# Kernel tuning notes

Measured on AMD Instinct MI355X. Metric: run time of the kernel, lower is better.

Reference implementation:

```python
import jax, jax.numpy as jnp
import numpy as np

N_NODES = 30000
N_EDGES = 480000
IN_CH, NF, OUT_CH = 64, 128, 3
N_HIDDEN = 6  # GCN(num_layers=7): conv0 (in->nf) + 6 convs (nf->nf)
SLOPE = 0.02


def setup_inputs() -> dict:
    key = jax.random.key(0)
    ks = jax.random.split(key, 8)
    x = jax.random.normal(ks[0], (N_NODES, IN_CH), dtype=jnp.float32)
    edge_index = jax.random.randint(ks[1], (2, N_EDGES), 0, N_NODES, dtype=jnp.int64)
    W0 = jax.random.normal(ks[2], (IN_CH, NF), dtype=jnp.float32) * (1.0 / np.sqrt(IN_CH))
    b0 = jnp.zeros((NF,), dtype=jnp.float32)
    Wh = jax.random.normal(ks[3], (N_HIDDEN, NF, NF), dtype=jnp.float32) * (1.0 / np.sqrt(NF))
    bh = jnp.zeros((N_HIDDEN, NF), dtype=jnp.float32)
    Wout = jax.random.normal(ks[4], (NF, OUT_CH), dtype=jnp.float32) * (1.0 / np.sqrt(NF))
    bout = jnp.zeros((OUT_CH,), dtype=jnp.float32)
    return {"x": x, "edge_index": edge_index, "W0": W0, "b0": b0,
            "Wh": Wh, "bh": bh, "Wout": Wout, "bout": bout}


def _gcn_norm(edge_index, n):
    # PyG GCNConv default: add self-loops, symmetric normalization D^-1/2 (A+I) D^-1/2
    loop = jnp.arange(n, dtype=edge_index.dtype)
    src = jnp.concatenate([edge_index[0], loop])
    dst = jnp.concatenate([edge_index[1], loop])
    deg = jax.ops.segment_sum(jnp.ones_like(dst, dtype=jnp.float32), dst, num_segments=n)
    dinv = jax.lax.rsqrt(deg)  # deg >= 1 due to self-loops
    norm = dinv[src] * dinv[dst]  # [E+N]
    return src, dst, norm


def _gcn_conv(h, W, b, src, dst, norm, n):
    h = h @ W                                   # [N, F_out]
    msg = h[src] * norm[:, None]                # gather + scale  [E+N, F_out]
    out = jax.ops.segment_sum(msg, dst, num_segments=n)  # scatter-add
    return out + b


def reference(x, edge_index, W0, b0, Wh, bh, Wout, bout):
    n = x.shape[0]
    src, dst, norm = _gcn_norm(edge_index, n)
    # 7-layer GCN stack with LeakyReLU(0.02) between layers; dropout is
    # identity in eval mode (training=False).
    h = _gcn_conv(x, W0, b0, src, dst, norm, n)
    for i in range(N_HIDDEN):
        h = jax.nn.leaky_relu(h, SLOPE)
        h = _gcn_conv(h, Wh[i], bh[i], src, dst, norm, n)
    # outer forward: leaky_relu -> dropout(eval=identity) -> out conv -> tanh*0.5
    h = jax.nn.leaky_relu(h, SLOPE)
    h = _gcn_conv(h, Wout, bout, src, dst, norm, n)
    return jnp.tanh(h) * 0.5
```

## Files before the change

kernel.cpp:

```cpp
#include <hip/hip_runtime.h>
#include <hip/hip_fp16.h>
#include <math.h>

#define NN 30000
#define NE 480000
#define NB 118
#define SCALE 512.0f
#define INVSCALE (1.0f / 512.0f)

typedef _Float16 half8 __attribute__((ext_vector_type(8)));
typedef float floatx4 __attribute__((ext_vector_type(4)));

__device__ __forceinline__ float lrelu(float v) { return v > 0.0f ? v : v * 0.02f; }

__device__ __forceinline__ float4 fma4(float4 v, float w, float4 a) {
    a.x = fmaf(v.x, w, a.x);
    a.y = fmaf(v.y, w, a.y);
    a.z = fmaf(v.z, w, a.z);
    a.w = fmaf(v.w, w, a.w);
    return a;
}

__device__ __forceinline__ float4 loadh4(const __half* p) {
    uint2 raw = *(const uint2*)p;
    __half2 h0 = *(__half2*)&raw.x;
    __half2 h1 = *(__half2*)&raw.y;
    float2 f0 = __half22float2(h0);
    float2 f1 = __half22float2(h1);
    return make_float4(f0.x, f0.y, f1.x, f1.y);
}


__global__ void k_count(const int* __restrict__ ei, int* __restrict__ cnt,
                        const float* __restrict__ W0, const float* __restrict__ Wh,
                        const float* __restrict__ b0, const float* __restrict__ bh,
                        __half* __restrict__ W0t, __half* __restrict__ Wht,
                        float* __restrict__ bs) {
    int g = blockIdx.x * 256 + threadIdx.x;
    if (g < NE) atomicAdd(&cnt[ei[NE + g]], 1);
    if (g < 8192) {
        int k = g >> 7, n = g & 127;
        W0t[n * 64 + k] = __float2half(W0[g] * SCALE);
    } else if (g < 8192 + 98304) {
        int j = g - 8192;
        int l = j >> 14;
        int r = j & 16383;
        int k = r >> 7, n = r & 127;
        Wht[l * 16384 + n * 128 + k] = __float2half(Wh[j]);
    } else if (g < 8192 + 98304 + 896) {
        int j = g - 8192 - 98304;
        bs[j] = (j < 128 ? b0[j] : bh[j - 128]) * SCALE;
    }
}

__global__ void k_scan1(const int* __restrict__ cnt, int* __restrict__ bsum,
                        float* __restrict__ dinv) {
    __shared__ int sd[256];
    int tid = threadIdx.x;
    int i = blockIdx.x * 256 + tid;
    int v = (i < NN) ? cnt[i] : 0;
    if (i < NN) dinv[i] = 1.0f / sqrtf((float)(v + 1));
    sd[tid] = v;
    __syncthreads();
    for (int off = 128; off > 0; off >>= 1) {
        if (tid < off) sd[tid] += sd[tid + off];
        __syncthreads();
    }
    if (tid == 0) bsum[blockIdx.x] = sd[0];
}

__global__ void k_scan3(const int* __restrict__ cnt, const int* __restrict__ bsum,
                        int* __restrict__ row_ptr, int* __restrict__ cursor) {
    __shared__ int sd[256];
    __shared__ int offs[128];
    int tid = threadIdx.x;
    if (tid < 128) offs[tid] = (tid < blockIdx.x) ? bsum[tid] : 0;
    __syncthreads();
    for (int o = 64; o > 0; o >>= 1) {
        if (tid < o) offs[tid] += offs[tid + o];
        __syncthreads();
    }
    int i = blockIdx.x * 256 + tid;
    int v = (i < NN) ? cnt[i] : 0;
    sd[tid] = v;
    __syncthreads();
    for (int off = 1; off < 256; off <<= 1) {
        int t = (tid >= off) ? sd[tid - off] : 0;
        __syncthreads();
        sd[tid] += t;
        __syncthreads();
    }
    if (i < NN) {
        int excl = offs[0] + sd[tid] - v;
        row_ptr[i] = excl;
        cursor[i] = excl;
        if (i == NN - 1) row_ptr[NN] = excl + v;
    }
}

__global__ void k_fill(const int* __restrict__ ei, const float* __restrict__ dinv,
                       int* __restrict__ cursor, int2* __restrict__ csr) {
    int e = blockIdx.x * 256 + threadIdx.x;
    if (e < NE) {
        int s = ei[e];
        int d = ei[NE + e];
        int pos = atomicAdd(&cursor[d], 1);
        float w = dinv[s] * dinv[d];
        csr[pos] = make_int2(s, __float_as_int(w));
    }
}


__launch_bounds__(512)
__global__ void k_layer0(const float* __restrict__ x, const int* __restrict__ row_ptr,
                         const int2* __restrict__ csr, const float* __restrict__ dinv,
                         const __half* __restrict__ Wt, const float* __restrict__ bias,
                         __half* __restrict__ out16) {
    __shared__ _Float16 hsF[2 * 4 * 16 * 8];
    int tid = threadIdx.x;
    int node0 = blockIdx.x * 16;
    {
        int nl = tid >> 5;
        int node = node0 + nl;
        int c = (tid & 31) * 2;
        float di = dinv[node];
        float w0 = di * di;
        float2 hv = *(const float2*)&x[(size_t)node * 64 + c];
        float2 acc[8];
        acc[0] = make_float2(hv.x * w0, hv.y * w0);
        #pragma unroll
        for (int j = 1; j < 8; j++) acc[j] = make_float2(0.f, 0.f);
        int e = row_ptr[node];
        int e1 = row_ptr[node + 1];
        for (; e + 8 <= e1; e += 8) {
            int2 sw[8];
            #pragma unroll
            for (int j = 0; j < 8; j++) sw[j] = csr[e + j];
            float2 v[8];
            #pragma unroll
            for (int j = 0; j < 8; j++) v[j] = *(const float2*)&x[(size_t)sw[j].x * 64 + c];
            #pragma unroll
            for (int j = 0; j < 8; j++) {
                float w = __int_as_float(sw[j].y);
                acc[j].x = fmaf(v[j].x, w, acc[j].x);
                acc[j].y = fmaf(v[j].y, w, acc[j].y);
            }
        }
        for (; e < e1; ++e) {
            int2 sw = csr[e];
            float2 v = *(const float2*)&x[(size_t)sw.x * 64 + c];
            float w = __int_as_float(sw.y);
            acc[0].x = fmaf(v.x, w, acc[0].x);
            acc[0].y = fmaf(v.y, w, acc[0].y);
        }
        #pragma unroll
        for (int j = 1; j < 8; j++) { acc[0].x += acc[j].x; acc[0].y += acc[j].y; }
        int ks = c >> 5, quad = (c >> 3) & 3, jj = c & 7;
        __half2 p = __floats2half2_rn(acc[0].x, acc[0].y);
        *(__half2*)&hsF[((ks * 4 + quad) * 16 + nl) * 8 + jj] = p;
    }
    __syncthreads();
    int wave = tid >> 6, lane = tid & 63, quad = lane >> 4, ln = lane & 15;
    half8 afrag[2];
    #pragma unroll
    for (int ks = 0; ks < 2; ks++)
        afrag[ks] = *(const half8*)&hsF[((ks * 4 + quad) * 16 + ln) * 8];
    floatx4 acc = (floatx4){0.f, 0.f, 0.f, 0.f};
    #pragma unroll
    for (int ks = 0; ks < 2; ks++) {
        half8 b = *(const half8*)&Wt[(size_t)(wave * 16 + ln) * 64 + ks * 32 + quad * 8];
        acc = __builtin_amdgcn_mfma_f32_16x16x32_f16(afrag[ks], b, acc, 0, 0, 0);
    }
    int col = wave * 16 + ln;
    float bb = bias[col];
    #pragma unroll
    for (int r = 0; r < 4; r++) {
        int row = node0 + quad * 4 + r;
        out16[(size_t)row * 128 + col] = __float2half(lrelu(acc[r] + bb));
    }
}

__launch_bounds__(512)
__global__ void k_layer_h(const __half* __restrict__ h, const int* __restrict__ row_ptr,
                          const int2* __restrict__ csr, const float* __restrict__ dinv,
                          const __half* __restrict__ Wt, const float* __restrict__ bias,
                          __half* __restrict__ out16) {
    __shared__ _Float16 hsF[4 * 4 * 16 * 8];
    int tid = threadIdx.x;
    int node0 = blockIdx.x * 16;
    {
        int nl = tid >> 5;
        int node = node0 + nl;
        int c = (tid & 31) * 4;
        float di = dinv[node];
        float w0 = di * di;
        float4 hv = loadh4(&h[(size_t)node * 128 + c]);
        float4 acc[8];
        acc[0] = make_float4(hv.x * w0, hv.y * w0, hv.z * w0, hv.w * w0);
        #pragma unroll
        for (int j = 1; j < 8; j++) acc[j] = make_float4(0.f, 0.f, 0.f, 0.f);
        int e = row_ptr[node];
        int e1 = row_ptr[node + 1];
        for (; e + 8 <= e1; e += 8) {
            int2 sw[8];
            #pragma unroll
            for (int j = 0; j < 8; j++) sw[j] = csr[e + j];
            float4 v[8];
            #pragma unroll
            for (int j = 0; j < 8; j++) v[j] = loadh4(&h[(size_t)sw[j].x * 128 + c]);
            #pragma unroll
            for (int j = 0; j < 8; j++) acc[j] = fma4(v[j], __int_as_float(sw[j].y), acc[j]);
        }
        for (; e < e1; ++e) {
            int2 sw = csr[e];
            float4 v = loadh4(&h[(size_t)sw.x * 128 + c]);
            acc[0] = fma4(v, __int_as_float(sw.y), acc[0]);
        }
        #pragma unroll
        for (int j = 1; j < 8; j++) {
            acc[0].x += acc[j].x;
            acc[0].y += acc[j].y;
            acc[0].z += acc[j].z;
            acc[0].w += acc[j].w;
        }
        int ks = c >> 5, quad = (c >> 3) & 3, jj = c & 7;
        __half2 p0 = __floats2half2_rn(acc[0].x, acc[0].y);
        __half2 p1 = __floats2half2_rn(acc[0].z, acc[0].w);
        uint2 pk;
        pk.x = *(unsigned int*)&p0;
        pk.y = *(unsigned int*)&p1;
        *(uint2*)&hsF[((ks * 4 + quad) * 16 + nl) * 8 + jj] = pk;
    }
    __syncthreads();
    int wave = tid >> 6, lane = tid & 63, quad = lane >> 4, ln = lane & 15;
    half8 afrag[4];
    #pragma unroll
    for (int ks = 0; ks < 4; ks++)
        afrag[ks] = *(const half8*)&hsF[((ks * 4 + quad) * 16 + ln) * 8];
    floatx4 acc = (floatx4){0.f, 0.f, 0.f, 0.f};
    #pragma unroll
    for (int ks = 0; ks < 4; ks++) {
        half8 b = *(const half8*)&Wt[(size_t)(wave * 16 + ln) * 128 + ks * 32 + quad * 8];
        acc = __builtin_amdgcn_mfma_f32_16x16x32_f16(afrag[ks], b, acc, 0, 0, 0);
    }
    int col = wave * 16 + ln;
    float bb = bias[col];
    #pragma unroll
    for (int r = 0; r < 4; r++) {
        int row = node0 + quad * 4 + r;
        out16[(size_t)row * 128 + col] = __float2half(lrelu(acc[r] + bb));
    }
}


__launch_bounds__(256)
__global__ void k_out_gemm(const __half* __restrict__ h, const float* __restrict__ Wout,
                           float* __restrict__ u) {
    __shared__ float Ws[128 * 3];
    int tid = threadIdx.x;
    for (int i = tid; i < 384; i += 256) Ws[i] = Wout[i];
    __syncthreads();
    int row = blockIdx.x * 8 + (tid >> 5);
    int lane = tid & 31;
    if (row >= NN) return;
    float4 v = loadh4(&h[(size_t)row * 128 + lane * 4]);
    int k = lane * 4;
    float a0 = v.x * Ws[k * 3 + 0] + v.y * Ws[(k + 1) * 3 + 0] +
               v.z * Ws[(k + 2) * 3 + 0] + v.w * Ws[(k + 3) * 3 + 0];
    float a1 = v.x * Ws[k * 3 + 1] + v.y * Ws[(k + 1) * 3 + 1] +
               v.z * Ws[(k + 2) * 3 + 1] + v.w * Ws[(k + 3) * 3 + 1];
    float a2 = v.x * Ws[k * 3 + 2] + v.y * Ws[(k + 1) * 3 + 2] +
               v.z * Ws[(k + 2) * 3 + 2] + v.w * Ws[(k + 3) * 3 + 2];
    for (int off = 16; off > 0; off >>= 1) {
        a0 += __shfl_down(a0, off, 32);
        a1 += __shfl_down(a1, off, 32);
        a2 += __shfl_down(a2, off, 32);
    }
    if (lane == 0) {
        u[(size_t)row * 3 + 0] = a0;
        u[(size_t)row * 3 + 1] = a1;
        u[(size_t)row * 3 + 2] = a2;
    }
}


__global__ void k_agg_out(const float* __restrict__ u, const int* __restrict__ row_ptr,
                          const int2* __restrict__ csr, const float* __restrict__ dinv,
                          const float* __restrict__ bout, float* __restrict__ out) {
    int node = blockIdx.x * 256 + threadIdx.x;
    if (node >= NN) return;
    float di = dinv[node], w0 = di * di;
    float s0 = u[(size_t)node * 3 + 0] * w0;
    float s1 = u[(size_t)node * 3 + 1] * w0;
    float s2 = u[(size_t)node * 3 + 2] * w0;
    float b0a = 0.f, b1a = 0.f, b2a = 0.f;
    int e = row_ptr[node];
    int e1 = row_ptr[node + 1];
    for (; e + 2 <= e1; e += 2) {
        int2 swa = csr[e], swb = csr[e + 1];
        float wa = __int_as_float(swa.y), wb = __int_as_float(swb.y);
        const float* ua = &u[(size_t)swa.x * 3];
        const float* ub = &u[(size_t)swb.x * 3];
        s0 = fmaf(ua[0], wa, s0);
        s1 = fmaf(ua[1], wa, s1);
        s2 = fmaf(ua[2], wa, s2);
        b0a = fmaf(ub[0], wb, b0a);
        b1a = fmaf(ub[1], wb, b1a);
        b2a = fmaf(ub[2], wb, b2a);
    }
    for (; e < e1; ++e) {
        int2 sw = csr[e];
        float w = __int_as_float(sw.y);
        const float* us = &u[(size_t)sw.x * 3];
        s0 = fmaf(us[0], w, s0);
        s1 = fmaf(us[1], w, s1);
        s2 = fmaf(us[2], w, s2);
    }
    out[(size_t)node * 3 + 0] = tanhf((s0 + b0a) * INVSCALE + bout[0]) * 0.5f;
    out[(size_t)node * 3 + 1] = tanhf((s1 + b1a) * INVSCALE + bout[1]) * 0.5f;
    out[(size_t)node * 3 + 2] = tanhf((s2 + b2a) * INVSCALE + bout[2]) * 0.5f;
}


extern "C" void kernel_launch(void* const* d_in, const int* in_sizes, int n_in,
                              void* d_out, int out_size, void* d_ws, size_t ws_size,
                              hipStream_t stream) {
    const float* x        = (const float*)d_in[0];
    const int*   ei       = (const int*)d_in[1];
    const float* W0       = (const float*)d_in[2];
    const float* b0       = (const float*)d_in[3];
    const float* Wh       = (const float*)d_in[4];
    const float* bh       = (const float*)d_in[5];
    const float* Wout     = (const float*)d_in[6];
    const float* bout     = (const float*)d_in[7];
    float* out            = (float*)d_out;

    char* ws = (char*)d_ws;
    float*  bufA   = (float*)(ws + 0);
    __half* bufB16 = (__half*)(ws + 15360000);
    __half* bufC16 = (__half*)(ws + 23040000);
    __half* W0t16  = (__half*)(ws + 30720000);
    __half* Wht16  = (__half*)(ws + 30736384);
    float*  bs     = (float*)(ws + 30932992);
    float*  dinv   = (float*)(ws + 30936576);
    int*    cnt    = (int*)  (ws + 31056576);
    int*    row_ptr= (int*)  (ws + 31176576);
    int*    cursor = (int*)  (ws + 31296640);
    int2*   csr    = (int2*) (ws + 31416640);

    int* bsum = (int*)bufA;

    hipMemsetAsync(cnt, 0, NN * sizeof(int), stream);
    k_count<<<(NE + 255) / 256, 256, 0, stream>>>(ei, cnt, W0, Wh, b0, bh, W0t16, Wht16, bs);
    k_scan1<<<NB, 256, 0, stream>>>(cnt, bsum, dinv);
    k_scan3<<<NB, 256, 0, stream>>>(cnt, bsum, row_ptr, cursor);
    k_fill<<<(NE + 255) / 256, 256, 0, stream>>>(ei, dinv, cursor, csr);

    k_layer0<<<NN / 16, 512, 0, stream>>>(x, row_ptr, csr, dinv, W0t16, bs, bufB16);

    __half* hin = bufB16;
    __half* hout = bufC16;
    for (int i = 0; i < 6; i++) {
        k_layer_h<<<NN / 16, 512, 0, stream>>>(hin, row_ptr, csr, dinv,
                                               Wht16 + (size_t)i * 16384,
                                               bs + 128 + (size_t)i * 128, hout);
        __half* t = hin; hin = hout; hout = t;
    }

    k_out_gemm<<<(NN + 7) / 8, 256, 0, stream>>>(hin, Wout, bufA );
    k_agg_out<<<(NN + 255) / 256, 256, 0, stream>>>(bufA, row_ptr, csr, dinv, bout, out);
}
```

Before: 368.5 us.

## Widen gather loads, halve block size, convert input features to fp16

```diff
diff --git a/kernel.cpp b/kernel.cpp
--- a/kernel.cpp
+++ b/kernel.cpp
@@ -30,14 +30,34 @@
     return make_float4(f0.x, f0.y, f1.x, f1.y);
 }
 
+__device__ __forceinline__ void loadh8(const __half* p, float4* lo, float4* hi) {
+    uint4 raw = *(const uint4*)p;
+    float2 f0 = __half22float2(*(__half2*)&raw.x);
+    float2 f1 = __half22float2(*(__half2*)&raw.y);
+    float2 f2 = __half22float2(*(__half2*)&raw.z);
+    float2 f3 = __half22float2(*(__half2*)&raw.w);
+    *lo = make_float4(f0.x, f0.y, f1.x, f1.y);
+    *hi = make_float4(f2.x, f2.y, f3.x, f3.y);
+}
+
 
 __global__ void k_count(const int* __restrict__ ei, int* __restrict__ cnt,
                         const float* __restrict__ W0, const float* __restrict__ Wh,
                         const float* __restrict__ b0, const float* __restrict__ bh,
+                        const float* __restrict__ x,
                         __half* __restrict__ W0t, __half* __restrict__ Wht,
-                        float* __restrict__ bs) {
+                        float* __restrict__ bs, __half* __restrict__ x16) {
     int g = blockIdx.x * 256 + threadIdx.x;
     if (g < NE) atomicAdd(&cnt[ei[NE + g]], 1);
+    {
+        float4 v = *(const float4*)&x[(size_t)g * 4];
+        __half2 a = __floats2half2_rn(v.x, v.y);
+        __half2 b = __floats2half2_rn(v.z, v.w);
+        uint2 pk;
+        pk.x = *(unsigned int*)&a;
+        pk.y = *(unsigned int*)&b;
+        *(uint2*)&x16[(size_t)g * 4] = pk;
+    }
     if (g < 8192) {
         int k = g >> 7, n = g & 127;
         W0t[n * 64 + k] = __float2half(W0[g] * SCALE);
@@ -111,8 +131,8 @@
 }
 
 
-__launch_bounds__(512)
-__global__ void k_layer0(const float* __restrict__ x, const int* __restrict__ row_ptr,
+__launch_bounds__(256)
+__global__ void k_layer0(const __half* __restrict__ x, const int* __restrict__ row_ptr,
                          const int2* __restrict__ csr, const float* __restrict__ dinv,
                          const __half* __restrict__ Wt, const float* __restrict__ bias,
                          __half* __restrict__ out16) {
@@ -120,44 +140,47 @@
     int tid = threadIdx.x;
     int node0 = blockIdx.x * 16;
     {
-        int nl = tid >> 5;
+        int nl = tid >> 4;
         int node = node0 + nl;
-        int c = (tid & 31) * 2;
+        int c = (tid & 15) * 4;
         float di = dinv[node];
         float w0 = di * di;
-        float2 hv = *(const float2*)&x[(size_t)node * 64 + c];
-        float2 acc[8];
-        acc[0] = make_float2(hv.x * w0, hv.y * w0);
-        #pragma unroll
-        for (int j = 1; j < 8; j++) acc[j] = make_float2(0.f, 0.f);
+        float4 hv = loadh4(&x[(size_t)node * 64 + c]);
+        float4 acc[8];
+        acc[0] = make_float4(hv.x * w0, hv.y * w0, hv.z * w0, hv.w * w0);
+        #pragma unroll
+        for (int j = 1; j < 8; j++) acc[j] = make_float4(0.f, 0.f, 0.f, 0.f);
         int e = row_ptr[node];
         int e1 = row_ptr[node + 1];
         for (; e + 8 <= e1; e += 8) {
             int2 sw[8];
             #pragma unroll
             for (int j = 0; j < 8; j++) sw[j] = csr[e + j];
-            float2 v[8];
-            #pragma unroll
-            for (int j = 0; j < 8; j++) v[j] = *(const float2*)&x[(size_t)sw[j].x * 64 + c];
-            #pragma unroll
-            for (int j = 0; j < 8; j++) {
-                float w = __int_as_float(sw[j].y);
-                acc[j].x = fmaf(v[j].x, w, acc[j].x);
-                acc[j].y = fmaf(v[j].y, w, acc[j].y);
-            }
+            float4 v[8];
+            #pragma unroll
+            for (int j = 0; j < 8; j++) v[j] = loadh4(&x[(size_t)sw[j].x * 64 + c]);
+            #pragma unroll
+            for (int j = 0; j < 8; j++) acc[j] = fma4(v[j], __int_as_float(sw[j].y), acc[j]);
         }
         for (; e < e1; ++e) {
             int2 sw = csr[e];
-            float2 v = *(const float2*)&x[(size_t)sw.x * 64 + c];
-            float w = __int_as_float(sw.y);
-            acc[0].x = fmaf(v.x, w, acc[0].x);
-            acc[0].y = fmaf(v.y, w, acc[0].y);
-        }
-        #pragma unroll
-        for (int j = 1; j < 8; j++) { acc[0].x += acc[j].x; acc[0].y += acc[j].y; }
+            float4 v = loadh4(&x[(size_t)sw.x * 64 + c]);
+            acc[0] = fma4(v, __int_as_float(sw.y), acc[0]);
+        }
+        #pragma unroll
+        for (int j = 1; j < 8; j++) {
+            acc[0].x += acc[j].x;
+            acc[0].y += acc[j].y;
+            acc[0].z += acc[j].z;
+            acc[0].w += acc[j].w;
+        }
         int ks = c >> 5, quad = (c >> 3) & 3, jj = c & 7;
-        __half2 p = __floats2half2_rn(acc[0].x, acc[0].y);
-        *(__half2*)&hsF[((ks * 4 + quad) * 16 + nl) * 8 + jj] = p;
+        __half2 p0 = __floats2half2_rn(acc[0].x, acc[0].y);
+        __half2 p1 = __floats2half2_rn(acc[0].z, acc[0].w);
+        uint2 pk;
+        pk.x = *(unsigned int*)&p0;
+        pk.y = *(unsigned int*)&p1;
+        *(uint2*)&hsF[((ks * 4 + quad) * 16 + nl) * 8 + jj] = pk;
     }
     __syncthreads();
     int wave = tid >> 6, lane = tid & 63, quad = lane >> 4, ln = lane & 15;
@@ -165,22 +188,26 @@
     #pragma unroll
     for (int ks = 0; ks < 2; ks++)
         afrag[ks] = *(const half8*)&hsF[((ks * 4 + quad) * 16 + ln) * 8];
-    floatx4 acc = (floatx4){0.f, 0.f, 0.f, 0.f};
     #pragma unroll
-    for (int ks = 0; ks < 2; ks++) {
-        half8 b = *(const half8*)&Wt[(size_t)(wave * 16 + ln) * 64 + ks * 32 + quad * 8];
-        acc = __builtin_amdgcn_mfma_f32_16x16x32_f16(afrag[ks], b, acc, 0, 0, 0);
-    }
-    int col = wave * 16 + ln;
-    float bb = bias[col];
-    #pragma unroll
-    for (int r = 0; r < 4; r++) {
-        int row = node0 + quad * 4 + r;
-        out16[(size_t)row * 128 + col] = __float2half(lrelu(acc[r] + bb));
-    }
-}
-
-__launch_bounds__(512)
+    for (int tc = 0; tc < 2; tc++) {
+        int tt = wave + tc * 4;
+        floatx4 acc = (floatx4){0.f, 0.f, 0.f, 0.f};
+        #pragma unroll
+        for (int ks = 0; ks < 2; ks++) {
+            half8 b = *(const half8*)&Wt[(size_t)(tt * 16 + ln) * 64 + ks * 32 + quad * 8];
+            acc = __builtin_amdgcn_mfma_f32_16x16x32_f16(afrag[ks], b, acc, 0, 0, 0);
+        }
+        int col = tt * 16 + ln;
+        float bb = bias[col];
+        #pragma unroll
+        for (int r = 0; r < 4; r++) {
+            int row = node0 + quad * 4 + r;
+            out16[(size_t)row * 128 + col] = __float2half(lrelu(acc[r] + bb));
+        }
+    }
+}
+
+__launch_bounds__(256)
 __global__ void k_layer_h(const __half* __restrict__ h, const int* __restrict__ row_ptr,
                           const int2* __restrict__ csr, const float* __restrict__ dinv,
                           const __half* __restrict__ Wt, const float* __restrict__ bias,
@@ -189,47 +216,64 @@
     int tid = threadIdx.x;
     int node0 = blockIdx.x * 16;
     {
-        int nl = tid >> 5;
+        int nl = tid >> 4;
         int node = node0 + nl;
-        int c = (tid & 31) * 4;
+        int c = (tid & 15) * 8;
         float di = dinv[node];
         float w0 = di * di;
-        float4 hv = loadh4(&h[(size_t)node * 128 + c]);
-        float4 acc[8];
-        acc[0] = make_float4(hv.x * w0, hv.y * w0, hv.z * w0, hv.w * w0);
-        #pragma unroll
-        for (int j = 1; j < 8; j++) acc[j] = make_float4(0.f, 0.f, 0.f, 0.f);
+        float4 hlo, hhi;
+        loadh8(&h[(size_t)node * 128 + c], &hlo, &hhi);
+        float4 acc[4][2];
+        acc[0][0] = make_float4(hlo.x * w0, hlo.y * w0, hlo.z * w0, hlo.w * w0);
+        acc[0][1] = make_float4(hhi.x * w0, hhi.y * w0, hhi.z * w0, hhi.w * w0);
+        #pragma unroll
+        for (int j = 1; j < 4; j++) {
+            acc[j][0] = make_float4(0.f, 0.f, 0.f, 0.f);
+            acc[j][1] = make_float4(0.f, 0.f, 0.f, 0.f);
+        }
         int e = row_ptr[node];
         int e1 = row_ptr[node + 1];
-        for (; e + 8 <= e1; e += 8) {
-            int2 sw[8];
-            #pragma unroll
-            for (int j = 0; j < 8; j++) sw[j] = csr[e + j];
-            float4 v[8];
-            #pragma unroll
-            for (int j = 0; j < 8; j++) v[j] = loadh4(&h[(size_t)sw[j].x * 128 + c]);
-            #pragma unroll
-            for (int j = 0; j < 8; j++) acc[j] = fma4(v[j], __int_as_float(sw[j].y), acc[j]);
+        for (; e + 4 <= e1; e += 4) {
+            int2 sw[4];
+            #pragma unroll
+            for (int j = 0; j < 4; j++) sw[j] = csr[e + j];
+            float4 vlo[4], vhi[4];
+            #pragma unroll
+            for (int j = 0; j < 4; j++)
+                loadh8(&h[(size_t)sw[j].x * 128 + c], &vlo[j], &vhi[j]);
+            #pragma unroll
+            for (int j = 0; j < 4; j++) {
+                float w = __int_as_float(sw[j].y);
+                acc[j][0] = fma4(vlo[j], w, acc[j][0]);
+                acc[j][1] = fma4(vhi[j], w, acc[j][1]);
+            }
         }
         for (; e < e1; ++e) {
             int2 sw = csr[e];
-            float4 v = loadh4(&h[(size_t)sw.x * 128 + c]);
-            acc[0] = fma4(v, __int_as_float(sw.y), acc[0]);
-        }
-        #pragma unroll
-        for (int j = 1; j < 8; j++) {
-            acc[0].x += acc[j].x;
-            acc[0].y += acc[j].y;
-            acc[0].z += acc[j].z;
-            acc[0].w += acc[j].w;
-        }
-        int ks = c >> 5, quad = (c >> 3) & 3, jj = c & 7;
-        __half2 p0 = __floats2half2_rn(acc[0].x, acc[0].y);
-        __half2 p1 = __floats2half2_rn(acc[0].z, acc[0].w);
-        uint2 pk;
+            float4 vlo, vhi;
+            loadh8(&h[(size_t)sw.x * 128 + c], &vlo, &vhi);
+            float w = __int_as_float(sw.y);
+            acc[0][0] = fma4(vlo, w, acc[0][0]);
+            acc[0][1] = fma4(vhi, w, acc[0][1]);
+        }
+        #pragma unroll
+        for (int j = 1; j < 4; j++) {
+            acc[0][0].x += acc[j][0].x; acc[0][0].y += acc[j][0].y;
+            acc[0][0].z += acc[j][0].z; acc[0][0].w += acc[j][0].w;
+            acc[0][1].x += acc[j][1].x; acc[0][1].y += acc[j][1].y;
+            acc[0][1].z += acc[j][1].z; acc[0][1].w += acc[j][1].w;
+        }
+        int ks = c >> 5, quad = (c >> 3) & 3;
+        __half2 p0 = __floats2half2_rn(acc[0][0].x, acc[0][0].y);
+        __half2 p1 = __floats2half2_rn(acc[0][0].z, acc[0][0].w);
+        __half2 p2 = __floats2half2_rn(acc[0][1].x, acc[0][1].y);
+        __half2 p3 = __floats2half2_rn(acc[0][1].z, acc[0][1].w);
+        uint4 pk;
         pk.x = *(unsigned int*)&p0;
         pk.y = *(unsigned int*)&p1;
-        *(uint2*)&hsF[((ks * 4 + quad) * 16 + nl) * 8 + jj] = pk;
+        pk.z = *(unsigned int*)&p2;
+        pk.w = *(unsigned int*)&p3;
+        *(uint4*)&hsF[((ks * 4 + quad) * 16 + nl) * 8] = pk;
     }
     __syncthreads();
     int wave = tid >> 6, lane = tid & 63, quad = lane >> 4, ln = lane & 15;
@@ -237,18 +281,22 @@
     #pragma unroll
     for (int ks = 0; ks < 4; ks++)
         afrag[ks] = *(const half8*)&hsF[((ks * 4 + quad) * 16 + ln) * 8];
-    floatx4 acc = (floatx4){0.f, 0.f, 0.f, 0.f};
     #pragma unroll
-    for (int ks = 0; ks < 4; ks++) {
-        half8 b = *(const half8*)&Wt[(size_t)(wave * 16 + ln) * 128 + ks * 32 + quad * 8];
-        acc = __builtin_amdgcn_mfma_f32_16x16x32_f16(afrag[ks], b, acc, 0, 0, 0);
-    }
-    int col = wave * 16 + ln;
-    float bb = bias[col];
-    #pragma unroll
-    for (int r = 0; r < 4; r++) {
-        int row = node0 + quad * 4 + r;
-        out16[(size_t)row * 128 + col] = __float2half(lrelu(acc[r] + bb));
+    for (int tc = 0; tc < 2; tc++) {
+        int tt = wave + tc * 4;
+        floatx4 acc = (floatx4){0.f, 0.f, 0.f, 0.f};
+        #pragma unroll
+        for (int ks = 0; ks < 4; ks++) {
+            half8 b = *(const half8*)&Wt[(size_t)(tt * 16 + ln) * 128 + ks * 32 + quad * 8];
+            acc = __builtin_amdgcn_mfma_f32_16x16x32_f16(afrag[ks], b, acc, 0, 0, 0);
+        }
+        int col = tt * 16 + ln;
+        float bb = bias[col];
+        #pragma unroll
+        for (int r = 0; r < 4; r++) {
+            int row = node0 + quad * 4 + r;
+            out16[(size_t)row * 128 + col] = __float2half(lrelu(acc[r] + bb));
+        }
     }
 }
 
@@ -339,29 +387,31 @@
     float*  bufA   = (float*)(ws + 0);
     __half* bufB16 = (__half*)(ws + 15360000);
     __half* bufC16 = (__half*)(ws + 23040000);
-    __half* W0t16  = (__half*)(ws + 30720000);
-    __half* Wht16  = (__half*)(ws + 30736384);
-    float*  bs     = (float*)(ws + 30932992);
-    float*  dinv   = (float*)(ws + 30936576);
-    int*    cnt    = (int*)  (ws + 31056576);
-    int*    row_ptr= (int*)  (ws + 31176576);
-    int*    cursor = (int*)  (ws + 31296640);
-    int2*   csr    = (int2*) (ws + 31416640);
+    __half* x16    = (__half*)(ws + 30720000);
+    __half* W0t16  = (__half*)(ws + 34560000);
+    __half* Wht16  = (__half*)(ws + 34576384);
+    float*  bs     = (float*)(ws + 34772992);
+    float*  dinv   = (float*)(ws + 34776576);
+    int*    cnt    = (int*)  (ws + 34896576);
+    int*    row_ptr= (int*)  (ws + 35016576);
+    int*    cursor = (int*)  (ws + 35136640);
+    int2*   csr    = (int2*) (ws + 35256640);
 
     int* bsum = (int*)bufA;
 
     hipMemsetAsync(cnt, 0, NN * sizeof(int), stream);
-    k_count<<<(NE + 255) / 256, 256, 0, stream>>>(ei, cnt, W0, Wh, b0, bh, W0t16, Wht16, bs);
+    k_count<<<(NE + 255) / 256, 256, 0, stream>>>(ei, cnt, W0, Wh, b0, bh, x,
+                                                  W0t16, Wht16, bs, x16);
     k_scan1<<<NB, 256, 0, stream>>>(cnt, bsum, dinv);
     k_scan3<<<NB, 256, 0, stream>>>(cnt, bsum, row_ptr, cursor);
     k_fill<<<(NE + 255) / 256, 256, 0, stream>>>(ei, dinv, cursor, csr);
 
-    k_layer0<<<NN / 16, 512, 0, stream>>>(x, row_ptr, csr, dinv, W0t16, bs, bufB16);
+    k_layer0<<<NN / 16, 256, 0, stream>>>(x16, row_ptr, csr, dinv, W0t16, bs, bufB16);
 
     __half* hin = bufB16;
     __half* hout = bufC16;
     for (int i = 0; i < 6; i++) {
-        k_layer_h<<<NN / 16, 512, 0, stream>>>(hin, row_ptr, csr, dinv,
+        k_layer_h<<<NN / 16, 256, 0, stream>>>(hin, row_ptr, csr, dinv,
                                                Wht16 + (size_t)i * 16384,
                                                bs + 128 + (size_t)i * 128, hout);
         __half* t = hin; hin = hout; hout = t;
```

Measured after the change: 323.2 us. 12.3% less time.
